# Optimization experiments

Measured on AMD Instinct MI355X. Metric: run time of the kernel, lower is better.

The kernel has to match this reference:

```python
import jax, jax.numpy as jnp
import numpy as np

EPS = 1e-5  # PNA std-aggregator epsilon
N_NODES, N_EDGES, F_DIM, N_LAYERS = 50000, 800000, 64, 3


def setup_inputs() -> dict:
    key = jax.random.key(0)
    ks = jax.random.split(key, 6)
    x = jax.random.normal(ks[0], (N_NODES, F_DIM), jnp.float32)
    edge_index = jax.random.randint(ks[1], (2, N_EDGES), 0, N_NODES, jnp.int32)
    # Per-layer parameters, stacked on a leading layer axis.
    pre_w = jax.random.normal(ks[2], (N_LAYERS, 2 * F_DIM, F_DIM), jnp.float32) / np.sqrt(2 * F_DIM).astype(np.float32)
    pre_b = jnp.zeros((N_LAYERS, F_DIM), jnp.float32)
    post_w = jax.random.normal(ks[3], (N_LAYERS, 13 * F_DIM, F_DIM), jnp.float32) / np.sqrt(13 * F_DIM).astype(np.float32)
    post_b = jnp.zeros((N_LAYERS, F_DIM), jnp.float32)
    lin_w = jax.random.normal(ks[4], (N_LAYERS, F_DIM, F_DIM), jnp.float32) / np.sqrt(F_DIM).astype(np.float32)
    lin_b = jnpp = jnp.zeros((N_LAYERS, F_DIM), jnp.float32)
    return dict(x=x, edge_index=edge_index, pre_w=pre_w, pre_b=pre_b,
                post_w=post_w, post_b=post_b, lin_w=lin_w, lin_b=lin_b)


def reference(x, edge_index, pre_w, pre_b, post_w, post_b, lin_w, lin_b):
    src, dst = edge_index[0], edge_index[1]
    n = x.shape[0]
    # In-degree of aggregation targets (clamped to >=1, as in PyG DegreeScalerAggregation).
    deg = jax.ops.segment_sum(jnp.ones_like(dst, dtype=x.dtype), dst, num_segments=n)
    has_edge = (deg > 0)[:, None]
    deg_c = jnp.maximum(deg, 1.0)[:, None]              # [N,1]
    log_deg = jnp.log(deg_c + 1.0)                      # [N,1]
    avg_log = jnp.mean(log_deg)
    amp = log_deg / avg_log                              # amplification scaler
    att = avg_log / log_deg                              # attenuation scaler

    h = x
    for l in range(pre_w.shape[0]):
        # message: pre_nn(cat([x_i, x_j]))  -> [E, F]
        m = jnp.concatenate([h[dst], h[src]], axis=-1) @ pre_w[l] + pre_b[l]
        # fused multi-aggregator scatter-reduce per target node
        s1 = jax.ops.segment_sum(m, dst, num_segments=n)
        s2 = jax.ops.segment_sum(m * m, dst, num_segments=n)
        mean = s1 / deg_c
        std = jnp.sqrt(jax.nn.relu(s2 / deg_c - mean * mean) + EPS)
        mx = jnp.where(has_edge, jax.ops.segment_max(m, dst, num_segments=n), 0.0)
        mn = jnp.where(has_edge, jax.ops.segment_min(m, dst, num_segments=n), 0.0)
        agg = jnp.concatenate([mean, mx, mn, std], axis=-1)        # [N, 4F]
        scaled = jnp.concatenate([agg, agg * amp, agg * att], -1)  # [N, 12F]
        # post_nn(cat([x, scaled])) then final lin, plus residual shortcut
        out = jnp.concatenate([h, scaled], axis=-1) @ post_w[l] + post_b[l]
        out = out @ lin_w[l] + lin_b[l]
        h = out + h
    return h
```

## Files before the change

### kernel.cpp

```cpp
#include <hip/hip_runtime.h>
#include <math.h>

#define EPSV 1e-5f
#define EPB3 4096
#define NBP 256
#define CAP 6144
#define CAPS (CAP + 768)

typedef short s16x8 __attribute__((ext_vector_type(8)));
typedef float f32x4 __attribute__((ext_vector_type(4)));
typedef float f32x2 __attribute__((ext_vector_type(2)));
typedef unsigned short u16;
typedef unsigned short u16x4 __attribute__((ext_vector_type(4)));

#define MFMA(a, b, c) __builtin_amdgcn_mfma_f32_16x16x32_bf16(a, b, c, 0, 0, 0)

__device__ inline u16 f2bf(float f) {
    unsigned u = __float_as_uint(f);
    return (u16)((u + 0x7FFF + ((u >> 16) & 1)) >> 16);
}
__device__ inline float bf2f(u16 h) { return __uint_as_float(((unsigned)h) << 16); }

__device__ inline void split8(const float4& a, const float4& b, s16x8& hv, s16x8& lv) {
    float f[8] = {a.x, a.y, a.z, a.w, b.x, b.y, b.z, b.w};
#pragma unroll
    for (int i = 0; i < 8; ++i) {
        u16 h = f2bf(f[i]);
        hv[i] = (short)h;
        lv[i] = (short)f2bf(f[i] - bf2f(h));
    }
}

typedef const __attribute__((address_space(1))) unsigned int* gp_t;
typedef __attribute__((address_space(3))) unsigned int* lp_t;
__device__ inline void gll(const void* g, void* l) {
    __builtin_amdgcn_global_load_lds((gp_t)g, (lp_t)l, 16, 0, 0);
}

__device__ inline int swzi(int r, int s) { return r * 64 + ((s ^ (r & 7)) << 3); }

__global__ __launch_bounds__(512) void k_pre1(
    const int* __restrict__ src, const int* __restrict__ dst, int E,
    int* __restrict__ bucketCursor, unsigned* __restrict__ edgeTmp,
    const float* __restrict__ pre_w, const float* __restrict__ post_w,
    const float* __restrict__ post_b, const float* __restrict__ lin_w,
    const float* __restrict__ lin_b, u16* __restrict__ WpT_hi,
    u16* __restrict__ WpT_lo, u16* __restrict__ WT_hi, u16* __restrict__ WT_lo,
    float* __restrict__ bpp, int NB1) {
    __shared__ int cnt[NBP], loff[NBP], lpos[NBP], gbase[NBP], sbuf[NBP];
    __shared__ unsigned stage[EPB3];
    int t = threadIdx.x;
    if ((int)blockIdx.x < NB1) {
        int base = blockIdx.x * EPB3;
        int cntE = min(EPB3, E - base);
        if (t < NBP) cnt[t] = 0;
        __syncthreads();
        unsigned ed[8];
#pragma unroll
        for (int j = 0; j < 8; ++j) {
            int idx = j * 512 + t;
            if (idx < cntE) {
                int e = base + idx;
                unsigned s = (unsigned)src[e];
                unsigned d = (unsigned)dst[e];
                ed[j] = ((d >> 8) << 24) | ((d & 255u) << 16) | s;
                atomicAdd(&cnt[d >> 8], 1);
            } else ed[j] = 0xFFFFFFFFu;
        }
        __syncthreads();
        if (t < NBP) sbuf[t] = cnt[t];
        __syncthreads();
        for (int o = 1; o < NBP; o <<= 1) {
            int v = 0;
            if (t < NBP && t >= o) v = sbuf[t - o];
            __syncthreads();
            if (t < NBP) sbuf[t] += v;
            __syncthreads();
        }
        if (t < NBP) {
            loff[t] = sbuf[t] - cnt[t];
            lpos[t] = sbuf[t] - cnt[t];
            gbase[t] = (cnt[t] > 0) ? atomicAdd(&bucketCursor[t], cnt[t]) : 0;
        }
        __syncthreads();
#pragma unroll
        for (int j = 0; j < 8; ++j) {
            if (ed[j] != 0xFFFFFFFFu) {
                int b = ed[j] >> 24;
                int p = atomicAdd(&lpos[b], 1);
                stage[p] = ed[j];
            }
        }
        __syncthreads();
        for (int i = t; i < cntE; i += 512) {
            unsigned pr = stage[i];
            int b = pr >> 24;
            int pos = gbase[b] + (i - loff[b]);
            if (pos < CAP) edgeTmp[(size_t)b * CAP + pos] = pr;
        }
        return;
    }
    int wq = blockIdx.x - NB1;
    int l = wq / 449;
    int bx = wq - l * 449;
    if (bx < 320) {
        if (t < 192) {
            int k = bx, j = t;
            int third = j >> 6, c = j & 63;
            float out = 0.f;
            int r = -1;
            if (k < 64) r = (third == 0) ? k : -1;
            else        r = 64 + third * 256 + (k - 64);
            if (r >= 0) {
                const float* pw = post_w + (size_t)(l * 832 + r) * 64;
                const float* lw = lin_w + (size_t)l * 64 * 64;
                float s = 0.f;
                for (int kk = 0; kk < 64; ++kk) s += pw[kk] * lw[kk * 64 + c];
                out = s;
            }
            u16 h = f2bf(out);
            size_t o = ((size_t)l * 192 + j) * 320 + k;
            WT_hi[o] = h;
            WT_lo[o] = f2bf(out - bf2f(h));
        }
    } else if (bx < 448) {
        if (t < 64) {
            int c = bx - 320, k = t;
            float v = pre_w[(size_t)l * 8192 + (size_t)(k + (c >= 64 ? 64 : 0)) * 64 + (c & 63)];
            u16 h = f2bf(v);
            size_t o = ((size_t)l * 128 + c) * 64 + k;
            WpT_hi[o] = h;
            WpT_lo[o] = f2bf(v - bf2f(h));
        }
    } else {
        if (t < 64) {
            int c = t;
            const float* pb = post_b + l * 64;
            const float* lw = lin_w + (size_t)l * 64 * 64;
            float s = lin_b[l * 64 + c];
            for (int k = 0; k < 64; ++k) s += pb[k] * lw[k * 64 + c];
            bpp[l * 64 + c] = s;
        }
    }
}

__global__ __launch_bounds__(512) void k_pre2(
    const unsigned* __restrict__ edgeTmp, const int* __restrict__ bucketCur,
    int* __restrict__ deg, int* __restrict__ offs, float* __restrict__ lsum,
    u16* __restrict__ srcSorted,
    const float* __restrict__ x, const u16* __restrict__ WpT_hi,
    const u16* __restrict__ WpT_lo, const float* __restrict__ pre_b,
    u16* __restrict__ Ph, u16* __restrict__ Qh,
    int N, int E, int NB) {
    __shared__ __align__(16) char smem[55296];
    int t = threadIdx.x;
    if ((int)blockIdx.x < NB) {
        int* scnt = (int*)smem;
        int* sbuf = (int*)(smem + 1024);
        int* lcur = (int*)(smem + 2048);
        int* lofs = (int*)(smem + 3072);
        float* fred = (float*)(smem + 4096);
        u16* stageSrc = (u16*)(smem + 5120);
        int* cntPs = (int*)(smem + 5120 + CAPS * 2);
        int b = blockIdx.x;
        int n0 = b << 8;
        int nodes = min(256, N - n0);
        if (t < NBP) { lcur[t] = 0; scnt[t] = 0; }
        __syncthreads();
        int cnt = min(bucketCur[b], CAP);
        const unsigned* ebase = edgeTmp + (size_t)b * CAP;
        for (int i = t; i < cnt; i += 512) atomicAdd(&lcur[(ebase[i] >> 16) & 255], 1);
        __syncthreads();
        float ls = 0.f;
        int d = 0, dP = 0;
        if (t < nodes) {
            d = lcur[t];
            deg[n0 + t] = d;
            ls = logf(fmaxf((float)d, 1.f) + 1.f);
            dP = (d + 3) & ~3;
        }
        if (t < 256) fred[t] = ls;
        if (t < NBP) sbuf[t] = dP;
        __syncthreads();
        for (int o = 1; o < NBP; o <<= 1) {
            int v = 0;
            if (t < NBP && t >= o) v = sbuf[t - o];
            __syncthreads();
            if (t < NBP) sbuf[t] += v;
            __syncthreads();
        }
        if (t < NBP) lofs[t] = sbuf[t] - dP;
        if (t < nodes) offs[n0 + t] = b * CAPS + (sbuf[t] - dP);
        if (t == NBP - 1) *cntPs = sbuf[t];
        __syncthreads();
        for (int o = 128; o > 0; o >>= 1) {
            if (t < o) fred[t] += fred[t + o];
            __syncthreads();
        }
        if (t == 0) atomicAdd(lsum, fred[0]);
        for (int i = t; i < cnt; i += 512) {
            unsigned p = ebase[i];
            int dl = (p >> 16) & 255;
            int r = atomicAdd(&scnt[dl], 1);
            stageSrc[lofs[dl] + r] = (u16)(p & 0xFFFFu);
        }
        __syncthreads();
        if (t < nodes && (d & 3)) {
            int lp = lofs[t];
            u16 lastv = stageSrc[lp + d - 1];
            for (int k = d; k < dP; ++k) stageSrc[lp + k] = lastv;
        }
        __syncthreads();
        int cntP = *cntPs;
        for (int i = t; i < cntP; i += 512) srcSorted[(size_t)b * CAPS + i] = stageSrc[i];
        return;
    }
    u16* Ah = (u16*)smem;
    u16* Al = (u16*)(smem + 9216);
    u16* Bh = (u16*)(smem + 18432);
    u16* Bl = (u16*)(smem + 36864);
    int rows0 = ((int)blockIdx.x - NB) * 64;
    int wid = t >> 6, lane = t & 63;
    int quad = lane >> 4, l16 = lane & 15;
    int wm = wid & 1, wn = wid >> 1;
    if (t < 256) {
#pragma unroll
        for (int it = 0; it < 2; ++it) {
            int task = it * 256 + t;
            int r = task >> 3, seg = task & 7;
            int row = rows0 + r;
            float4 v0 = make_float4(0.f, 0.f, 0.f, 0.f), v1 = v0;
            if (row < N) {
                v0 = *(const float4*)&x[(size_t)row * 64 + seg * 8];
                v1 = *(const float4*)&x[(size_t)row * 64 + seg * 8 + 4];
            }
            s16x8 hv, lv;
            split8(v0, v1, hv, lv);
            *(s16x8*)&Ah[r * 72 + seg * 8] = hv;
            *(s16x8*)&Al[r * 72 + seg * 8] = lv;
        }
#pragma unroll
        for (int it = 0; it < 4; ++it) {
            int task = it * 256 + t;
            int c = task >> 3, seg = task & 7;
            *(s16x8*)&Bh[c * 72 + seg * 8] = *(const s16x8*)&WpT_hi[(size_t)c * 64 + seg * 8];
            *(s16x8*)&Bl[c * 72 + seg * 8] = *(const s16x8*)&WpT_lo[(size_t)c * 64 + seg * 8];
        }
    }
    __syncthreads();
    if (t < 256) {
        f32x4 acc[2][4];
#pragma unroll
        for (int mt = 0; mt < 2; ++mt)
#pragma unroll
            for (int tt = 0; tt < 4; ++tt) acc[mt][tt] = (f32x4){0.f, 0.f, 0.f, 0.f};
#pragma unroll
        for (int c = 0; c < 2; ++c) {
            s16x8 ah[2], al[2];
#pragma unroll
            for (int mt = 0; mt < 2; ++mt) {
                int r = wm * 32 + mt * 16 + l16;
                ah[mt] = *(s16x8*)&Ah[r * 72 + c * 32 + quad * 8];
                al[mt] = *(s16x8*)&Al[r * 72 + c * 32 + quad * 8];
            }
#pragma unroll
            for (int tt = 0; tt < 4; ++tt) {
                int cc = wn * 64 + tt * 16 + l16;
                s16x8 bh = *(s16x8*)&Bh[cc * 72 + c * 32 + quad * 8];
                s16x8 bl = *(s16x8*)&Bl[cc * 72 + c * 32 + quad * 8];
#pragma unroll
                for (int mt = 0; mt < 2; ++mt) {
                    acc[mt][tt] = MFMA(ah[mt], bh, acc[mt][tt]);
                    acc[mt][tt] = MFMA(ah[mt], bl, acc[mt][tt]);
                    if (wn == 0) acc[mt][tt] = MFMA(al[mt], bh, acc[mt][tt]);
                }
            }
        }
#pragma unroll
        for (int mt = 0; mt < 2; ++mt)
#pragma unroll
            for (int tt = 0; tt < 4; ++tt) {
                int col = wn * 64 + tt * 16 + l16;
#pragma unroll
                for (int r = 0; r < 4; ++r) {
                    int row = rows0 + wm * 32 + mt * 16 + quad * 4 + r;
                    if (row >= N) continue;
                    float v = acc[mt][tt][r];
                    if (col < 64) Ph[(size_t)row * 64 + col] = f2bf(v + pre_b[col]);
                    else          Qh[(size_t)row * 64 + (col - 64)] = f2bf(v);
                }
            }
    }
}


__global__ __launch_bounds__(256) void k_agg(const u16* __restrict__ Ph,
                                             const u16* __restrict__ Qh,
                                             const int* __restrict__ offs,
                                             const int* __restrict__ degp,
                                             const u16* __restrict__ ss,
                                             u16* __restrict__ AGGh, int N) {
    int w = threadIdx.x >> 6, lane = threadIdx.x & 63;
    int g = lane >> 4;
    int f4b = (lane & 15) << 3;
    int node = blockIdx.x * 16 + w * 4 + g;
    int nc = min(node, N - 1);
    int beg = offs[nc];
    int d = (node < N) ? degp[nc] : 0;
    int dP = (d + 3) & ~3;
    int end = beg + dP;
    int mdP = dP;
    mdP = max(mdP, __shfl_xor(mdP, 16));
    mdP = max(mdP, __shfl_xor(mdP, 32));
    int trips = mdP >> 2;

    f32x2 sum01 = {0.f, 0.f}, sum23 = {0.f, 0.f};
    f32x2 sq01 = {0.f, 0.f}, sq23 = {0.f, 0.f};
    f32x2 mx01 = {-3.4e38f, -3.4e38f}, mx23 = {-3.4e38f, -3.4e38f};
    f32x2 mn01 = {3.4e38f, 3.4e38f}, mn23 = {3.4e38f, 3.4e38f};

    const char* qbase = (const char*)Qh;

#define ACC4(LO, HI)                                                        \
    {                                                                       \
        f32x2 fa, fb;                                                       \
        fa.x = __uint_as_float((LO) << 16);                                 \
        fa.y = __uint_as_float((LO) & 0xFFFF0000u);                         \
        fb.x = __uint_as_float((HI) << 16);                                 \
        fb.y = __uint_as_float((HI) & 0xFFFF0000u);                         \
        sum01 += fa; sq01 = __builtin_elementwise_fma(fa, fa, sq01);        \
        mx01 = __builtin_elementwise_max(mx01, fa);                         \
        mn01 = __builtin_elementwise_min(mn01, fa);                         \
        sum23 += fb; sq23 = __builtin_elementwise_fma(fb, fb, sq23);        \
        mx23 = __builtin_elementwise_max(mx23, fb);                         \
        mn23 = __builtin_elementwise_min(mn23, fb);                         \
    }

    int e = beg;
    for (int it = 0; it < trips; ++it, e += 4) {
        if (e < end) {
            uint2 sw = *(const uint2*)(ss + e);
            unsigned a0 = ((sw.x & 0xFFFFu) << 7) | (unsigned)f4b;
            unsigned a1 = ((sw.x >> 16) << 7) | (unsigned)f4b;
            unsigned a2 = ((sw.y & 0xFFFFu) << 7) | (unsigned)f4b;
            unsigned a3 = ((sw.y >> 16) << 7) | (unsigned)f4b;
            uint2 qa = *(const uint2*)(qbase + a0);
            uint2 qb = *(const uint2*)(qbase + a1);
            uint2 qc = *(const uint2*)(qbase + a2);
            uint2 qd = *(const uint2*)(qbase + a3);
            ACC4(qa.x, qa.y);
            ACC4(qb.x, qb.y);
            ACC4(qc.x, qc.y);
            ACC4(qd.x, qd.y);
        }
    }
#undef ACC4

    if (d & 3) {
        unsigned sl = ss[beg + d - 1];
        uint2 ql = *(const uint2*)(qbase + ((sl << 7) | (unsigned)f4b));
        float padf = (float)(dP - d);
        f32x2 pf = {padf, padf};
        f32x2 fa, fb;
        fa.x = __uint_as_float(ql.x << 16);
        fa.y = __uint_as_float(ql.x & 0xFFFF0000u);
        fb.x = __uint_as_float(ql.y << 16);
        fb.y = __uint_as_float(ql.y & 0xFFFF0000u);
        f32x2 ta = pf * fa, tb = pf * fb;
        sum01 -= ta; sq01 = __builtin_elementwise_fma(-ta, fa, sq01);
        sum23 -= tb; sq23 = __builtin_elementwise_fma(-tb, fb, sq23);
    }

    float sum0 = sum01.x, sum1 = sum01.y, sum2 = sum23.x, sum3 = sum23.y;
    float sq0 = sq01.x, sq1 = sq01.y, sq2 = sq23.x, sq3 = sq23.y;
    float mx0 = mx01.x, mx1 = mx01.y, mx2 = mx23.x, mx3 = mx23.y;
    float mn0 = mn01.x, mn1 = mn01.y, mn2 = mn23.x, mn3 = mn23.y;

    float dc = fmaxf((float)d, 1.f);
    float inv = 1.0f / dc;
    float e0 = sum0 * inv, e1 = sum1 * inv, e2 = sum2 * inv, e3 = sum3 * inv;
    float sd0 = sqrtf(fmaxf(fmaf(-e0, e0, sq0 * inv), 0.f) + EPSV);
    float sd1 = sqrtf(fmaxf(fmaf(-e1, e1, sq1 * inv), 0.f) + EPSV);
    float sd2 = sqrtf(fmaxf(fmaf(-e2, e2, sq2 * inv), 0.f) + EPSV);
    float sd3 = sqrtf(fmaxf(fmaf(-e3, e3, sq3 * inv), 0.f) + EPSV);

    uint2 pw = *(const uint2*)((const char*)Ph + (((unsigned)nc << 7) | (unsigned)f4b));
    float p0 = __uint_as_float(pw.x << 16), p1 = __uint_as_float(pw.x & 0xFFFF0000u);
    float p2 = __uint_as_float(pw.y << 16), p3 = __uint_as_float(pw.y & 0xFFFF0000u);

    bool he = d > 0;
    float m0 = he ? p0 + e0 : 0.f, m1 = he ? p1 + e1 : 0.f;
    float m2 = he ? p2 + e2 : 0.f, m3 = he ? p3 + e3 : 0.f;
    float X0 = he ? p0 + mx0 : 0.f, X1 = he ? p1 + mx1 : 0.f;
    float X2 = he ? p2 + mx2 : 0.f, X3 = he ? p3 + mx3 : 0.f;
    float n0 = he ? p0 + mn0 : 0.f, n1 = he ? p1 + mn1 : 0.f;
    float n2 = he ? p2 + mn2 : 0.f, n3 = he ? p3 + mn3 : 0.f;

    if (node < N) {
        u16* out = (u16*)((char*)AGGh + (((unsigned)node << 9) | (unsigned)f4b));
        *(u16x4*)(out)       = (u16x4){f2bf(m0), f2bf(m1), f2bf(m2), f2bf(m3)};
        *(u16x4*)(out + 64)  = (u16x4){f2bf(X0), f2bf(X1), f2bf(X2), f2bf(X3)};
        *(u16x4*)(out + 128) = (u16x4){f2bf(n0), f2bf(n1), f2bf(n2), f2bf(n3)};
        *(u16x4*)(out + 192) = (u16x4){f2bf(sd0), f2bf(sd1), f2bf(sd2), f2bf(sd3)};
    }
}

__global__ __launch_bounds__(512) void k_gemm2(const float* __restrict__ hIn,
                                               const u16* __restrict__ AGGh,
                                               const u16* __restrict__ WT_hi,
                                               const u16* __restrict__ WT_lo,
                                               const float* __restrict__ bpp,
                                               const int* __restrict__ degp,
                                               const float* __restrict__ lsum,
                                               float* __restrict__ hOut,
                                               int doNext,
                                               const u16* __restrict__ WpN_hi,
                                               const u16* __restrict__ WpN_lo,
                                               const float* __restrict__ pre_bN,
                                               u16* __restrict__ PhN,
                                               u16* __restrict__ QhN, int M) {
    __shared__ __align__(16) u16 S[32768];
    const int AHo  = 0;
    const int ALo  = 8192;
    const int B1Ho = 16384;
    const int B1Lo = 20480;
    const int B2Ho = 8192;
    const int B2Lo = 20480;
    const int BCHo = 16384;
    const int BCLo = 24576;
    int t = threadIdx.x, wid = t >> 6, lane = t & 63;
    int rows0 = blockIdx.x * 128;
    int quad = lane >> 4, l16 = lane & 15;
    int wm = wid & 3, wn = wid >> 2;
    int lr8 = lane >> 3, ls = lane & 7;

    f32x4 acc[2][6];
#pragma unroll
    for (int mt = 0; mt < 2; ++mt)
#pragma unroll
        for (int tt = 0; tt < 6; ++tt) acc[mt][tt] = (f32x4){0.f, 0.f, 0.f, 0.f};

#pragma unroll
    for (int it = 0; it < 2; ++it) {
        int task = it * 512 + t;
        int r = task >> 3, seg = task & 7;
        int row = rows0 + r;
        float4 v0 = make_float4(0.f, 0.f, 0.f, 0.f), v1 = v0;
        if (row < M) {
            v0 = *(const float4*)&hIn[(size_t)row * 64 + seg * 8];
            v1 = *(const float4*)&hIn[(size_t)row * 64 + seg * 8 + 4];
        }
        s16x8 hv, lv;
        split8(v0, v1, hv, lv);
        *(s16x8*)&S[AHo + swzi(r, seg)] = hv;
        *(s16x8*)&S[ALo + swzi(r, seg)] = lv;
    }
    {
        int r = wid * 8 + lr8;
        int sx = ls ^ (r & 7);
        gll(WT_hi + (size_t)r * 320 + sx * 8, &S[B1Ho + wid * 512]);
        gll(WT_lo + (size_t)r * 320 + sx * 8, &S[B1Lo + wid * 512]);
    }
    __syncthreads();
#pragma unroll
    for (int half = 0; half < 2; ++half) {
        int s = half * 4 + quad;
        s16x8 ah[2], al[2];
#pragma unroll
        for (int mt = 0; mt < 2; ++mt) {
            int r = wm * 32 + mt * 16 + l16;
            ah[mt] = *(s16x8*)&S[AHo + swzi(r, s)];
            al[mt] = *(s16x8*)&S[ALo + swzi(r, s)];
        }
#pragma unroll
        for (int cg = 0; cg < 2; ++cg) {
            int cc = wn * 32 + cg * 16 + l16;
            s16x8 bh = *(s16x8*)&S[B1Ho + swzi(cc, s)];
            s16x8 bl = *(s16x8*)&S[B1Lo + swzi(cc, s)];
#pragma unroll
            for (int mt = 0; mt < 2; ++mt) {
                acc[mt][cg] = MFMA(ah[mt], bh, acc[mt][cg]);
                acc[mt][cg] = MFMA(al[mt], bh, acc[mt][cg]);
                acc[mt][cg] = MFMA(ah[mt], bl, acc[mt][cg]);
            }
        }
    }

    for (int chunk = 0; chunk < 4; ++chunk) {
        __syncthreads();
#pragma unroll
        for (int j = 0; j < 2; ++j) {
            int rb = (wid + j * 8) * 8;
            int r = rb + lr8;
            int rowc = min(rows0 + r, M - 1);
            int sx = ls ^ (r & 7);
            gll(AGGh + (size_t)rowc * 256 + chunk * 64 + sx * 8, &S[AHo + rb * 64]);
        }
#pragma unroll
        for (int j = 0; j < 3; ++j) {
            int rb = (wid * 3 + j) * 8;
            int r = rb + lr8;
            int sx = ls ^ (r & 7);
            size_t go = (size_t)r * 320 + 64 + chunk * 64 + sx * 8;
            gll(WT_hi + go, &S[B2Ho + rb * 64]);
            gll(WT_lo + go, &S[B2Lo + rb * 64]);
        }
        __syncthreads();
#pragma unroll
        for (int half = 0; half < 2; ++half) {
            int s = half * 4 + quad;
            s16x8 ah[2];
#pragma unroll
            for (int mt = 0; mt < 2; ++mt) {
                int r = wm * 32 + mt * 16 + l16;
                ah[mt] = *(s16x8*)&S[AHo + swzi(r, s)];
            }
#pragma unroll
            for (int tt = 0; tt < 6; ++tt) {
                int cc = wn * 32 + (tt & 1) * 16 + (tt >> 1) * 64 + l16;
                s16x8 bh = *(s16x8*)&S[B2Ho + swzi(cc, s)];
                s16x8 bl = *(s16x8*)&S[B2Lo + swzi(cc, s)];
#pragma unroll
                for (int mt = 0; mt < 2; ++mt) {
                    acc[mt][tt] = MFMA(ah[mt], bh, acc[mt][tt]);
                    acc[mt][tt] = MFMA(ah[mt], bl, acc[mt][tt]);
                }
            }
        }
    }

    float hv[2][2][4];
    float avg = *lsum / (float)M;
#pragma unroll
    for (int mt = 0; mt < 2; ++mt)
#pragma unroll
        for (int r = 0; r < 4; ++r) {
            int row = rows0 + wm * 32 + mt * 16 + quad * 4 + r;
            float am = 1.f, at = 1.f, hin0 = 0.f, hin1 = 0.f;
            if (row < M) {
                float dc = fmaxf((float)degp[row], 1.f);
                float ld = logf(dc + 1.f);
                am = ld / avg;
                at = avg / ld;
                hin0 = hIn[(size_t)row * 64 + wn * 32 + l16];
                hin1 = hIn[(size_t)row * 64 + wn * 32 + 16 + l16];
            }
#pragma unroll
            for (int cg = 0; cg < 2; ++cg) {
                int col = wn * 32 + cg * 16 + l16;
                float v = acc[mt][cg][r] + am * acc[mt][cg + 2][r] + at * acc[mt][cg + 4][r]
                        + (cg == 0 ? hin0 : hin1) + bpp[col];
                hv[mt][cg][r] = v;
                if (row < M) hOut[(size_t)row * 64 + col] = v;
            }
        }

    if (doNext) {
        __syncthreads();
#pragma unroll
        for (int j = 0; j < 2; ++j) {
            int rb = (wid + j * 8) * 8;
            int r = rb + lr8;
            int sx = ls ^ (r & 7);
            gll(WpN_hi + (size_t)r * 64 + sx * 8, &S[BCHo + rb * 64]);
            gll(WpN_lo + (size_t)r * 64 + sx * 8, &S[BCLo + rb * 64]);
        }
#pragma unroll
        for (int mt = 0; mt < 2; ++mt)
#pragma unroll
            for (int cg = 0; cg < 2; ++cg) {
                int lc = wn * 32 + cg * 16 + l16;
                int s = lc >> 3, b = lc & 7;
#pragma unroll
                for (int r = 0; r < 4; ++r) {
                    int rl = wm * 32 + mt * 16 + quad * 4 + r;
                    float v = hv[mt][cg][r];
                    u16 hi = f2bf(v);
                    int o = rl * 64 + ((s ^ (rl & 7)) << 3) + b;
                    S[AHo + o] = hi;
                    S[ALo + o] = f2bf(v - bf2f(hi));
                }
            }
        __syncthreads();

        f32x4 acc2[2][4];
#pragma unroll
        for (int mt = 0; mt < 2; ++mt)
#pragma unroll
            for (int tt = 0; tt < 4; ++tt) acc2[mt][tt] = (f32x4){0.f, 0.f, 0.f, 0.f};

#pragma unroll
        for (int half = 0; half < 2; ++half) {
            int s = half * 4 + quad;
            s16x8 ah[2], al[2];
#pragma unroll
            for (int mt = 0; mt < 2; ++mt) {
                int r = wm * 32 + mt * 16 + l16;
                ah[mt] = *(s16x8*)&S[AHo + swzi(r, s)];
                al[mt] = *(s16x8*)&S[ALo + swzi(r, s)];
            }
#pragma unroll
            for (int tt = 0; tt < 4; ++tt) {
                int cc = wn * 64 + tt * 16 + l16;
                s16x8 bh = *(s16x8*)&S[BCHo + swzi(cc, s)];
                s16x8 bl = *(s16x8*)&S[BCLo + swzi(cc, s)];
#pragma unroll
                for (int mt = 0; mt < 2; ++mt) {
                    acc2[mt][tt] = MFMA(ah[mt], bh, acc2[mt][tt]);
                    acc2[mt][tt] = MFMA(ah[mt], bl, acc2[mt][tt]);
                    if (wn == 0) acc2[mt][tt] = MFMA(al[mt], bh, acc2[mt][tt]);
                }
            }
        }

#pragma unroll
        for (int mt = 0; mt < 2; ++mt)
#pragma unroll
            for (int tt = 0; tt < 4; ++tt) {
                int col = wn * 64 + tt * 16 + l16;
#pragma unroll
                for (int r = 0; r < 4; ++r) {
                    int row = rows0 + wm * 32 + mt * 16 + quad * 4 + r;
                    if (row >= M) continue;
                    float v = acc2[mt][tt][r];
                    if (col < 64) PhN[(size_t)row * 64 + col] = f2bf(v + pre_bN[col]);
                    else          QhN[(size_t)row * 64 + (col - 64)] = f2bf(v);
                }
            }
    }
}


extern "C" void kernel_launch(void* const* d_in, const int* in_sizes, int n_in,
                              void* d_out, int out_size, void* d_ws, size_t ws_size,
                              hipStream_t stream) {
    const float* x      = (const float*)d_in[0];
    const int*   ei     = (const int*)d_in[1];
    const float* pre_w  = (const float*)d_in[2];
    const float* pre_b  = (const float*)d_in[3];
    const float* post_w = (const float*)d_in[4];
    const float* post_b = (const float*)d_in[5];
    const float* lin_w  = (const float*)d_in[6];
    const float* lin_b  = (const float*)d_in[7];

    const int N = in_sizes[0] / 64;
    const int E = in_sizes[1] / 2;
    const int L = in_sizes[2] / (128 * 64);

    const int* srcIdx = ei;
    const int* dstIdx = ei + E;

    char* ws = (char*)d_ws;
    size_t off = 0;
    auto alloc = [&](size_t bytes) {
        void* p = ws + off;
        off += (bytes + 255) & ~(size_t)255;
        return p;
    };
    int*      deg        = (int*)alloc((size_t)N * 4);
    int*      offs       = (int*)alloc((size_t)(N + 1) * 4);
    u16*      srcSorted  = (u16*)alloc((size_t)NBP * CAPS * 2);
    unsigned* edgeTmp    = (unsigned*)alloc((size_t)NBP * CAP * 4);
    int*      bucketCur  = (int*)alloc(NBP * 4);
    float*    lsum       = (float*)alloc(256);
    u16*      WpT_hi     = (u16*)alloc((size_t)L * 128 * 64 * 2);
    u16*      WpT_lo     = (u16*)alloc((size_t)L * 128 * 64 * 2);
    u16*      WT_hi      = (u16*)alloc((size_t)L * 192 * 320 * 2);
    u16*      WT_lo      = (u16*)alloc((size_t)L * 192 * 320 * 2);
    float*    bpp        = (float*)alloc((size_t)L * 64 * 4);
    u16*      Ph         = (u16*)alloc((size_t)N * 64 * 2);
    u16*      Qh         = (u16*)alloc((size_t)N * 64 * 2);
    u16*      AGGh       = (u16*)alloc((size_t)N * 256 * 2);
    float*    hA         = (float*)alloc((size_t)N * 64 * 4);
    float*    hB         = (float*)alloc((size_t)N * 64 * 4);
    (void)ws_size;

    int NB = (N + 255) >> 8;
    int NB1 = (E + EPB3 - 1) / EPB3;
    int gblk = (N + 63) / 64;
    int gblk2 = (N + 127) / 128;

    hipMemsetAsync(bucketCur, 0, NBP * 4, stream);
    hipMemsetAsync(lsum, 0, 4, stream);

    k_pre1<<<NB1 + 449 * L, 512, 0, stream>>>(
        srcIdx, dstIdx, E, bucketCur, edgeTmp,
        pre_w, post_w, post_b, lin_w, lin_b,
        WpT_hi, WpT_lo, WT_hi, WT_lo, bpp, NB1);

    k_pre2<<<NB + gblk, 512, 0, stream>>>(
        edgeTmp, bucketCur, deg, offs, lsum, srcSorted,
        x, WpT_hi, WpT_lo, pre_b, Ph, Qh, N, E, NB);

    const float* hIn = x;
    float* hbuf[2] = {hA, hB};
    for (int l = 0; l < L; ++l) {
        float* hOut = (l == L - 1) ? (float*)d_out : hbuf[l & 1];
        int dn = (l < L - 1) ? 1 : 0;
        int ln = dn ? (l + 1) : 0;
        k_agg<<<(N + 15) / 16, 256, 0, stream>>>(Ph, Qh, offs, deg, srcSorted, AGGh, N);
        k_gemm2<<<gblk2, 512, 0, stream>>>(hIn, AGGh,
                                           WT_hi + (size_t)l * 192 * 320,
                                           WT_lo + (size_t)l * 192 * 320,
                                           bpp + (size_t)l * 64,
                                           deg, lsum, hOut, dn,
                                           WpT_hi + (size_t)ln * 128 * 64,
                                           WpT_lo + (size_t)ln * 128 * 64,
                                           pre_b + (size_t)ln * 64,
                                           Ph, Qh, N);
        hIn = hOut;
    }
}
```

Baseline: 249.7 us.

## Double-buffer AGG and weight chunk loads in post-GEMM with explicit waitcnt fences

The k_gemm2 chunk loop becomes a software-pipelined, double-buffered sequence. Each chunk's global-to-LDS loads are issued before the previous chunk is computed, and the first chunk is prefetched ahead of the h-part GEMM. Fences use explicit vmcnt/lgkmcnt waits plus s_barrier instead of full __syncthreads, and the next layer's pre-weights are prefetched during the last chunk. LDS per block doubles to 128KB, which may cut occupancy to one 512-thread block per CU, and the hand-counted vmcnt values have to match the number of outstanding loads exactly.

```diff
diff --git a/kernel.cpp b/kernel.cpp
--- a/kernel.cpp
+++ b/kernel.cpp
@@ -405,6 +405,64 @@
     }
 }
 
+#define ISSUE_CHUNK(CH, AB, BHB, BLB)                                       \
+    {                                                                       \
+        _Pragma("unroll")                                                   \
+        for (int j = 0; j < 2; ++j) {                                       \
+            int rb = (wid + j * 8) * 8;                                     \
+            int r = rb + lr8;                                               \
+            int rowc = min(rows0 + r, M - 1);                               \
+            int sx = ls ^ (r & 7);                                          \
+            gll(AGGh + (size_t)rowc * 256 + (CH) * 64 + sx * 8, &S[(AB) + rb * 64]); \
+        }                                                                   \
+        _Pragma("unroll")                                                   \
+        for (int j = 0; j < 3; ++j) {                                       \
+            int rb = (wid * 3 + j) * 8;                                     \
+            int r = rb + lr8;                                               \
+            int sx = ls ^ (r & 7);                                          \
+            size_t go = (size_t)r * 320 + 64 + (CH) * 64 + sx * 8;          \
+            gll(WT_hi + go, &S[(BHB) + rb * 64]);                           \
+            gll(WT_lo + go, &S[(BLB) + rb * 64]);                           \
+        }                                                                   \
+    }
+
+#define COMPUTE_CHUNK(AB, BHB, BLB)                                         \
+    _Pragma("unroll")                                                       \
+    for (int half = 0; half < 2; ++half) {                                  \
+        int s = half * 4 + quad;                                            \
+        s16x8 ah[2];                                                        \
+        _Pragma("unroll")                                                   \
+        for (int mt = 0; mt < 2; ++mt) {                                    \
+            int r = wm * 32 + mt * 16 + l16;                                \
+            ah[mt] = *(s16x8*)&S[(AB) + swzi(r, s)];                        \
+        }                                                                   \
+        _Pragma("unroll")                                                   \
+        for (int tt = 0; tt < 6; ++tt) {                                    \
+            int cc = wn * 32 + (tt & 1) * 16 + (tt >> 1) * 64 + l16;        \
+            s16x8 bh = *(s16x8*)&S[(BHB) + swzi(cc, s)];                    \
+            s16x8 bl = *(s16x8*)&S[(BLB) + swzi(cc, s)];                    \
+            _Pragma("unroll")                                               \
+            for (int mt = 0; mt < 2; ++mt) {                                \
+                acc[mt][tt] = MFMA(ah[mt], bh, acc[mt][tt]);                \
+                acc[mt][tt] = MFMA(ah[mt], bl, acc[mt][tt]);                \
+            }                                                               \
+        }                                                                   \
+    }
+
+#define FENCE_VM(NSTR)                                                      \
+    __builtin_amdgcn_sched_barrier(0);                                      \
+    asm volatile("s_waitcnt vmcnt(" NSTR ")" ::: "memory");                 \
+    __builtin_amdgcn_sched_barrier(0);                                      \
+    __builtin_amdgcn_s_barrier();                                           \
+    __builtin_amdgcn_sched_barrier(0);
+
+#define FENCE_LG()                                                          \
+    __builtin_amdgcn_sched_barrier(0);                                      \
+    asm volatile("s_waitcnt lgkmcnt(0)" ::: "memory");                      \
+    __builtin_amdgcn_sched_barrier(0);                                      \
+    __builtin_amdgcn_s_barrier();                                           \
+    __builtin_amdgcn_sched_barrier(0);
+
 __global__ __launch_bounds__(512) void k_gemm2(const float* __restrict__ hIn,
                                                const u16* __restrict__ AGGh,
                                                const u16* __restrict__ WT_hi,
@@ -419,15 +477,10 @@
                                                const float* __restrict__ pre_bN,
                                                u16* __restrict__ PhN,
                                                u16* __restrict__ QhN, int M) {
-    __shared__ __align__(16) u16 S[32768];
-    const int AHo  = 0;
-    const int ALo  = 8192;
-    const int B1Ho = 16384;
-    const int B1Lo = 20480;
-    const int B2Ho = 8192;
-    const int B2Lo = 20480;
-    const int BCHo = 16384;
-    const int BCLo = 24576;
+    __shared__ __align__(16) u16 S[65536];
+    const int P1AH = 0, P1AL = 8192, P1BH = 16384, P1BL = 20480;
+    const int A1 = 0, B1H = 8192, B1L = 20480;
+    const int A0 = 32768, B0H = 40960, B0L = 53248;
     int t = threadIdx.x, wid = t >> 6, lane = t & 63;
     int rows0 = blockIdx.x * 128;
     int quad = lane >> 4, l16 = lane & 15;
@@ -439,6 +492,8 @@
     for (int mt = 0; mt < 2; ++mt)
 #pragma unroll
         for (int tt = 0; tt < 6; ++tt) acc[mt][tt] = (f32x4){0.f, 0.f, 0.f, 0.f};
+
+    ISSUE_CHUNK(0, A0, B0H, B0L)
 
 #pragma unroll
     for (int it = 0; it < 2; ++it) {
@@ -452,14 +507,14 @@
         }
         s16x8 hv, lv;
         split8(v0, v1, hv, lv);
-        *(s16x8*)&S[AHo + swzi(r, seg)] = hv;
-        *(s16x8*)&S[ALo + swzi(r, seg)] = lv;
+        *(s16x8*)&S[P1AH + swzi(r, seg)] = hv;
+        *(s16x8*)&S[P1AL + swzi(r, seg)] = lv;
     }
     {
         int r = wid * 8 + lr8;
         int sx = ls ^ (r & 7);
-        gll(WT_hi + (size_t)r * 320 + sx * 8, &S[B1Ho + wid * 512]);
-        gll(WT_lo + (size_t)r * 320 + sx * 8, &S[B1Lo + wid * 512]);
+        gll(WT_hi + (size_t)r * 320 + sx * 8, &S[P1BH + wid * 512]);
+        gll(WT_lo + (size_t)r * 320 + sx * 8, &S[P1BL + wid * 512]);
     }
     __syncthreads();
 #pragma unroll
@@ -469,14 +524,14 @@
 #pragma unroll
         for (int mt = 0; mt < 2; ++mt) {
             int r = wm * 32 + mt * 16 + l16;
-            ah[mt] = *(s16x8*)&S[AHo + swzi(r, s)];
-            al[mt] = *(s16x8*)&S[ALo + swzi(r, s)];
+            ah[mt] = *(s16x8*)&S[P1AH + swzi(r, s)];
+            al[mt] = *(s16x8*)&S[P1AL + swzi(r, s)];
         }
 #pragma unroll
         for (int cg = 0; cg < 2; ++cg) {
             int cc = wn * 32 + cg * 16 + l16;
-            s16x8 bh = *(s16x8*)&S[B1Ho + swzi(cc, s)];
-            s16x8 bl = *(s16x8*)&S[B1Lo + swzi(cc, s)];
+            s16x8 bh = *(s16x8*)&S[P1BH + swzi(cc, s)];
+            s16x8 bl = *(s16x8*)&S[P1BL + swzi(cc, s)];
 #pragma unroll
             for (int mt = 0; mt < 2; ++mt) {
                 acc[mt][cg] = MFMA(ah[mt], bh, acc[mt][cg]);
@@ -485,49 +540,35 @@
             }
         }
     }
-
-    for (int chunk = 0; chunk < 4; ++chunk) {
-        __syncthreads();
+    __syncthreads();
+
+    ISSUE_CHUNK(1, A1, B1H, B1L)
+    FENCE_VM("8")
+    COMPUTE_CHUNK(A0, B0H, B0L)
+    FENCE_LG()
+    ISSUE_CHUNK(2, A0, B0H, B0L)
+    FENCE_VM("8")
+    COMPUTE_CHUNK(A1, B1H, B1L)
+    FENCE_LG()
+    ISSUE_CHUNK(3, A1, B1H, B1L)
+    FENCE_VM("8")
+    COMPUTE_CHUNK(A0, B0H, B0L)
+    FENCE_LG()
+    if (doNext) {
 #pragma unroll
         for (int j = 0; j < 2; ++j) {
             int rb = (wid + j * 8) * 8;
             int r = rb + lr8;
-            int rowc = min(rows0 + r, M - 1);
             int sx = ls ^ (r & 7);
-            gll(AGGh + (size_t)rowc * 256 + chunk * 64 + sx * 8, &S[AHo + rb * 64]);
-        }
-#pragma unroll
-        for (int j = 0; j < 3; ++j) {
-            int rb = (wid * 3 + j) * 8;
-            int r = rb + lr8;
-            int sx = ls ^ (r & 7);
-            size_t go = (size_t)r * 320 + 64 + chunk * 64 + sx * 8;
-            gll(WT_hi + go, &S[B2Ho + rb * 64]);
-            gll(WT_lo + go, &S[B2Lo + rb * 64]);
-        }
-        __syncthreads();
-#pragma unroll
-        for (int half = 0; half < 2; ++half) {
-            int s = half * 4 + quad;
-            s16x8 ah[2];
-#pragma unroll
-            for (int mt = 0; mt < 2; ++mt) {
-                int r = wm * 32 + mt * 16 + l16;
-                ah[mt] = *(s16x8*)&S[AHo + swzi(r, s)];
-            }
-#pragma unroll
-            for (int tt = 0; tt < 6; ++tt) {
-                int cc = wn * 32 + (tt & 1) * 16 + (tt >> 1) * 64 + l16;
-                s16x8 bh = *(s16x8*)&S[B2Ho + swzi(cc, s)];
-                s16x8 bl = *(s16x8*)&S[B2Lo + swzi(cc, s)];
-#pragma unroll
-                for (int mt = 0; mt < 2; ++mt) {
-                    acc[mt][tt] = MFMA(ah[mt], bh, acc[mt][tt]);
-                    acc[mt][tt] = MFMA(ah[mt], bl, acc[mt][tt]);
-                }
-            }
-        }
-    }
+            gll(WpN_hi + (size_t)r * 64 + sx * 8, &S[B0H + rb * 64]);
+            gll(WpN_lo + (size_t)r * 64 + sx * 8, &S[B0L + rb * 64]);
+        }
+        FENCE_VM("4")
+    } else {
+        FENCE_VM("0")
+    }
+    COMPUTE_CHUNK(A1, B1H, B1L)
+    FENCE_LG()
 
     float hv[2][2][4];
     float avg = *lsum / (float)M;
@@ -556,15 +597,6 @@
         }
 
     if (doNext) {
-        __syncthreads();
-#pragma unroll
-        for (int j = 0; j < 2; ++j) {
-            int rb = (wid + j * 8) * 8;
-            int r = rb + lr8;
-            int sx = ls ^ (r & 7);
-            gll(WpN_hi + (size_t)r * 64 + sx * 8, &S[BCHo + rb * 64]);
-            gll(WpN_lo + (size_t)r * 64 + sx * 8, &S[BCLo + rb * 64]);
-        }
 #pragma unroll
         for (int mt = 0; mt < 2; ++mt)
 #pragma unroll
@@ -577,8 +609,8 @@
                     float v = hv[mt][cg][r];
                     u16 hi = f2bf(v);
                     int o = rl * 64 + ((s ^ (rl & 7)) << 3) + b;
-                    S[AHo + o] = hi;
-                    S[ALo + o] = f2bf(v - bf2f(hi));
+                    S[P1AH + o] = hi;
+                    S[P1AL + o] = f2bf(v - bf2f(hi));
                 }
             }
         __syncthreads();
@@ -596,14 +628,14 @@
 #pragma unroll
             for (int mt = 0; mt < 2; ++mt) {
                 int r = wm * 32 + mt * 16 + l16;
-                ah[mt] = *(s16x8*)&S[AHo + swzi(r, s)];
-                al[mt] = *(s16x8*)&S[ALo + swzi(r, s)];
+                ah[mt] = *(s16x8*)&S[P1AH + swzi(r, s)];
+                al[mt] = *(s16x8*)&S[P1AL + swzi(r, s)];
             }
 #pragma unroll
             for (int tt = 0; tt < 4; ++tt) {
                 int cc = wn * 64 + tt * 16 + l16;
-                s16x8 bh = *(s16x8*)&S[BCHo + swzi(cc, s)];
-                s16x8 bl = *(s16x8*)&S[BCLo + swzi(cc, s)];
+                s16x8 bh = *(s16x8*)&S[B0H + swzi(cc, s)];
+                s16x8 bl = *(s16x8*)&S[B0L + swzi(cc, s)];
 #pragma unroll
                 for (int mt = 0; mt < 2; ++mt) {
                     acc2[mt][tt] = MFMA(ah[mt], bh, acc2[mt][tt]);
```

Result: slower. 281.8 us (+12.9%).
